# Optimization experiments

Hardware: AMD Instinct MI355X
Metric: run time of the kernel (lower is better)

## Reference

```python
import math
import jax, jax.numpy as jnp
import numpy as np

B, S, D, H = 2, 2048, 1024, 16
Dh = D // H
EPS = 1e-5


def layernorm(x, g, b):
    mu = jnp.mean(x, axis=-1, keepdims=True)
    var = jnp.mean(jnp.square(x - mu), axis=-1, keepdims=True)
    return (x - mu) * jax.lax.rsqrt(var + EPS) * g + b


def setup_inputs() -> dict:
    key = jax.random.key(0)
    ks = jax.random.split(key, 8)
    sc = 0.02
    return {
        "x": jax.random.normal(ks[0], (B, S, D), jnp.float32),
        # per-head wq weights stacked: [H, D, Dh] (wk/wv are unused in the original)
        "wq_w": jax.random.normal(ks[1], (H, D, Dh), jnp.float32) * sc,
        "wq_b": jnp.zeros((H, Dh), jnp.float32),
        "fc_w": jax.random.normal(ks[2], (D, D), jnp.float32) * sc,
        "fc_b": jnp.zeros((D,), jnp.float32),
        "ln1_g": jnp.ones((D,), jnp.float32),
        "ln1_b": jnp.zeros((D,), jnp.float32),
        "w1": jax.random.normal(ks[3], (D, 4 * D), jnp.float32) * sc,
        "b1": jnp.zeros((4 * D,), jnp.float32),
        "w2": jax.random.normal(ks[4], (4 * D, D), jnp.float32) * sc,
        "b2": jnp.zeros((D,), jnp.float32),
        "ln2_g": jnp.ones((D,), jnp.float32),
        "ln2_b": jnp.zeros((D,), jnp.float32),
    }


def reference(x, wq_w, wq_b, fc_w, fc_b, ln1_g, ln1_b, w1, b1, w2, b2, ln2_g, ln2_b):
    # NOTE: original bug — wq is applied to q, k and v; since q=k=v=x, Q=K=V.
    qh = jnp.einsum("bsd,hde->bhse", x, wq_w) + wq_b[None, :, None, :]  # [B,H,S,Dh]
    scores = jnp.einsum("bhse,bhte->bhst", qh, qh) / math.sqrt(Dh)      # [B,H,S,S]
    attn = jax.nn.softmax(scores, axis=-1)
    ctx = jnp.einsum("bhst,bhte->bhse", attn, qh)                        # [B,H,S,Dh]
    # concat heads along last dim (head h -> columns h*Dh:(h+1)*Dh)
    y = jnp.transpose(ctx, (0, 2, 1, 3)).reshape(B, S, D)
    y = y @ fc_w + fc_b
    y = layernorm(y + x, ln1_g, ln1_b)
    y1 = jax.nn.relu(y @ w1 + b1) @ w2 + b2
    return layernorm(y + y1, ln2_g, ln2_b)
```

## Files before the change

kernel.cpp:

```cpp
#include <hip/hip_runtime.h>
#include <hip/hip_bf16.h>

typedef unsigned short u16;
typedef __bf16 bf16x8 __attribute__((ext_vector_type(8)));
typedef float floatx4 __attribute__((ext_vector_type(4)));

__device__ __forceinline__ float bf2f_u(u16 u) {
    union { unsigned int i; float f; } x; x.i = ((unsigned int)u) << 16; return x.f;
}
__device__ __forceinline__ u16 f2bf_u(float f) {
    union { float f; unsigned int i; } x; x.f = f;
    unsigned int r = x.i + 0x7fffu + ((x.i >> 16) & 1u);
    return (u16)(r >> 16);
}

__device__ __forceinline__ void gl_lds16(const void* g, void* l) {
    __builtin_amdgcn_global_load_lds(
        (const __attribute__((address_space(1))) void*)g,
        (__attribute__((address_space(3))) void*)l, 16, 0, 0);
}

__global__ __launch_bounds__(256) void tobf_k(const float* __restrict__ in,
                                              u16* __restrict__ out) {
    int i = (blockIdx.x * 256 + threadIdx.x) * 8;
    float4 v0 = *(const float4*)&in[i];
    float4 v1 = *(const float4*)&in[i + 4];
    u16 tmp[8] = {f2bf_u(v0.x), f2bf_u(v0.y), f2bf_u(v0.z), f2bf_u(v0.w),
                  f2bf_u(v1.x), f2bf_u(v1.y), f2bf_u(v1.z), f2bf_u(v1.w)};
    *(uint4*)&out[i] = *(const uint4*)tmp;
}

__global__ __launch_bounds__(256) void transpose_bf_k(
    const float* __restrict__ in, u16* __restrict__ out,
    int R, int C, size_t inZ, size_t outZ)
{
    __shared__ u16 T[64][80];
    const float* ip = in + blockIdx.z * inZ;
    u16* op = out + blockIdx.z * outZ;
    const int r0 = blockIdx.y * 64, c0 = blockIdx.x * 64;
    const int t = threadIdx.x;
#pragma unroll
    for (int i = 0; i < 4; i++) {
        int c = t + i * 256;
        int rr = c >> 4, cc = (c & 15) * 4;
        float4 v = *(const float4*)&ip[(size_t)(r0 + rr) * C + c0 + cc];
        T[cc + 0][rr] = f2bf_u(v.x); T[cc + 1][rr] = f2bf_u(v.y);
        T[cc + 2][rr] = f2bf_u(v.z); T[cc + 3][rr] = f2bf_u(v.w);
    }
    __syncthreads();
#pragma unroll
    for (int i = 0; i < 2; i++) {
        int c = t + i * 256;
        int oc = c >> 3, k8 = (c & 7) * 8;
        uint4 v = *(const uint4*)&T[oc][k8];
        *(uint4*)&op[(size_t)(c0 + oc) * R + r0 + k8] = v;
    }
}

__global__ __launch_bounds__(256) void transpose_qh_k(const u16* __restrict__ in,
                                                      u16* __restrict__ out)
{
    __shared__ u16 T[64][72];
    const int bh = blockIdx.y;
    const int s0 = blockIdx.x * 64;
    const u16* ip = in + (size_t)bh * (2048 * 64);
    u16* op = out + (size_t)bh * (64 * 2048);
    const int t = threadIdx.x;
#pragma unroll
    for (int i = 0; i < 2; i++) {
        int c = t + i * 256;
        int r = c >> 3, cc = (c & 7) * 8;
        uint4 v = *(const uint4*)&ip[(size_t)(s0 + r) * 64 + cc];
        const u16* pv = (const u16*)&v;
#pragma unroll
        for (int k = 0; k < 8; k++) T[cc + k][r] = pv[k];
    }
    __syncthreads();
#pragma unroll
    for (int i = 0; i < 2; i++) {
        int c = t + i * 256;
        int d = c >> 3, cs = (c & 7) * 8;
        uint4 v = *(const uint4*)&T[d][cs];
        *(uint4*)&op[(size_t)d * 2048 + s0 + cs] = v;
    }
}

__device__ __forceinline__ void gemm_epilogue(
    floatx4 (&acc)[4][2], int m0, int n0, int wm, int wn, int lr, int quad,
    int N, const float* __restrict__ bias, const u16* __restrict__ resid,
    float* __restrict__ out, u16* __restrict__ out_bf, int mode)
{
#pragma unroll
    for (int i = 0; i < 4; i++) {
#pragma unroll
        for (int j = 0; j < 2; j++) {
#pragma unroll
            for (int r = 0; r < 4; r++) {
                int grow = m0 + wm + i * 16 + quad * 4 + r;
                int gcol = n0 + wn + j * 16 + lr;
                float val = acc[i][j][r];
                if (bias) val += bias[gcol];
                if (mode == 0) {
                    int bb = grow >> 11, ss = grow & 2047;
                    int h = gcol >> 6, e = gcol & 63;
                    out_bf[(((size_t)bb * 16 + h) * 2048 + ss) * 64 + e] = f2bf_u(val);
                } else if (mode == 1) {
                    size_t idx = (size_t)grow * N + gcol;
                    out[idx] = val + bf2f_u(resid[idx]);
                } else if (mode == 2) {
                    out_bf[(size_t)grow * N + gcol] = f2bf_u(fmaxf(val, 0.f));
                } else if (mode == 3) {
                    size_t idx = (size_t)grow * N + gcol;
                    out[idx] = out[idx] + val;
                } else {
                    size_t idx = (size_t)grow * N + gcol;
                    out_bf[idx] = f2bf_u(val + bf2f_u(resid[idx]));
                }
            }
        }
    }
}

__global__ __launch_bounds__(256) void gemm_bt64_k(
    const u16* __restrict__ A, const u16* __restrict__ Bt,
    int gm, int gn, int N, int K, int ldb,
    const float* __restrict__ bias, const u16* __restrict__ resid,
    float* __restrict__ out, u16* __restrict__ out_bf, int mode)
{
    __shared__ __align__(16) u16 As[2][128 * 64];
    __shared__ __align__(16) u16 Bs[2][64 * 64];

    const int id = blockIdx.x;
    const int xcd = id & 7, s = id >> 3;
    const int bandM = gm >> 2, bandN = gn >> 1;
    const int m0 = ((xcd >> 1) * bandM + (s % bandM)) * 128;
    const int n0 = ((xcd & 1) * bandN + (s / bandM)) * 64;

    const int t = threadIdx.x;
    const int wid = t >> 6, lane = t & 63;
    const int wm = (wid >> 1) * 64, wn = (wid & 1) * 32;
    const int lr = lane & 15, quad = lane >> 4;
    const int srow = lane >> 3;
    const int scol = ((lane & 7) ^ (lane >> 3)) * 8;

    floatx4 acc[4][2];
#pragma unroll
    for (int i = 0; i < 4; i++)
#pragma unroll
        for (int j = 0; j < 2; j++)
            acc[i][j] = (floatx4){0.f, 0.f, 0.f, 0.f};

    auto stage = [&](int b, int k0) {
#pragma unroll
        for (int i = 0; i < 4; i++) {
            int rb = wid * 32 + i * 8;
            gl_lds16(&A[(size_t)(m0 + rb + srow) * K + k0 + scol], &As[b][rb * 64]);
        }
#pragma unroll
        for (int i = 0; i < 2; i++) {
            int rb = wid * 16 + i * 8;
            gl_lds16(&Bt[(size_t)(n0 + rb + srow) * ldb + k0 + scol], &Bs[b][rb * 64]);
        }
    };

    const int nt = K >> 6;
    stage(0, 0);

    int cur = 0;
    for (int tt = 0; tt < nt; tt++) {
        asm volatile("s_waitcnt vmcnt(0)" ::: "memory");
        __builtin_amdgcn_s_barrier();
        __builtin_amdgcn_sched_barrier(0);
        if (tt + 1 < nt) stage(cur ^ 1, (tt + 1) * 64);

#pragma unroll
        for (int kk = 0; kk < 2; kk++) {
            bf16x8 af[4], bfr[2];
#pragma unroll
            for (int i = 0; i < 4; i++) {
                int R = wm + i * 16 + lr;
                int c = ((kk * 4 + quad) ^ (lr & 7)) * 8;
                af[i] = *(const bf16x8*)&As[cur][R * 64 + c];
            }
#pragma unroll
            for (int j = 0; j < 2; j++) {
                int R = wn + j * 16 + lr;
                int c = ((kk * 4 + quad) ^ (lr & 7)) * 8;
                bfr[j] = *(const bf16x8*)&Bs[cur][R * 64 + c];
            }
#pragma unroll
            for (int i = 0; i < 4; i++)
#pragma unroll
                for (int j = 0; j < 2; j++)
                    acc[i][j] = __builtin_amdgcn_mfma_f32_16x16x32_bf16(af[i], bfr[j], acc[i][j], 0, 0, 0);
        }
        cur ^= 1;
    }

    gemm_epilogue(acc, m0, n0, wm, wn, lr, quad, N, bias, resid, out, out_bf, mode);
}

__global__ __launch_bounds__(256) void gemm_bt64p3_k(
    const u16* __restrict__ A, const u16* __restrict__ Bt,
    int gm, int gn, int N, int K, int ldb,
    const float* __restrict__ bias, const u16* __restrict__ resid,
    float* __restrict__ out, u16* __restrict__ out_bf, int mode)
{
    __shared__ __align__(16) u16 As[3][128 * 64];
    __shared__ __align__(16) u16 Bs[3][64 * 64];

    const int id = blockIdx.x;
    const int xcd = id & 7, s = id >> 3;
    const int bandM = gm >> 2, bandN = gn >> 1;
    const int m0 = ((xcd >> 1) * bandM + (s % bandM)) * 128;
    const int n0 = ((xcd & 1) * bandN + (s / bandM)) * 64;

    const int t = threadIdx.x;
    const int wid = t >> 6, lane = t & 63;
    const int wm = (wid >> 1) * 64, wn = (wid & 1) * 32;
    const int lr = lane & 15, quad = lane >> 4;
    const int srow = lane >> 3;
    const int scol = ((lane & 7) ^ (lane >> 3)) * 8;

    floatx4 acc[4][2];
#pragma unroll
    for (int i = 0; i < 4; i++)
#pragma unroll
        for (int j = 0; j < 2; j++)
            acc[i][j] = (floatx4){0.f, 0.f, 0.f, 0.f};

    auto stage = [&](int b, int k0) {
#pragma unroll
        for (int i = 0; i < 4; i++) {
            int rb = wid * 32 + i * 8;
            gl_lds16(&A[(size_t)(m0 + rb + srow) * K + k0 + scol], &As[b][rb * 64]);
        }
#pragma unroll
        for (int i = 0; i < 2; i++) {
            int rb = wid * 16 + i * 8;
            gl_lds16(&Bt[(size_t)(n0 + rb + srow) * ldb + k0 + scol], &Bs[b][rb * 64]);
        }
    };

    const int nt = K >> 6;
    stage(0, 0);
    stage(1, 64);

    int cur = 0, nxt = 2;
    for (int tt = 0; tt < nt; tt++) {
        if (tt + 1 < nt) asm volatile("s_waitcnt vmcnt(6)" ::: "memory");
        else             asm volatile("s_waitcnt vmcnt(0)" ::: "memory");
        __builtin_amdgcn_s_barrier();
        __builtin_amdgcn_sched_barrier(0);
        if (tt + 2 < nt) stage(nxt, (tt + 2) * 64);

#pragma unroll
        for (int kk = 0; kk < 2; kk++) {
            bf16x8 af[4], bfr[2];
#pragma unroll
            for (int i = 0; i < 4; i++) {
                int R = wm + i * 16 + lr;
                int c = ((kk * 4 + quad) ^ (lr & 7)) * 8;
                af[i] = *(const bf16x8*)&As[cur][R * 64 + c];
            }
#pragma unroll
            for (int j = 0; j < 2; j++) {
                int R = wn + j * 16 + lr;
                int c = ((kk * 4 + quad) ^ (lr & 7)) * 8;
                bfr[j] = *(const bf16x8*)&Bs[cur][R * 64 + c];
            }
#pragma unroll
            for (int i = 0; i < 4; i++)
#pragma unroll
                for (int j = 0; j < 2; j++)
                    acc[i][j] = __builtin_amdgcn_mfma_f32_16x16x32_bf16(af[i], bfr[j], acc[i][j], 0, 0, 0);
        }
        cur = (cur == 2) ? 0 : cur + 1;
        nxt = (nxt == 2) ? 0 : nxt + 1;
    }

    gemm_epilogue(acc, m0, n0, wm, wn, lr, quad, N, bias, resid, out, out_bf, mode);
}

#define PST 68
__global__ __launch_bounds__(256) void attn_mfma_k(const u16* __restrict__ qh,
                                                   const u16* __restrict__ qhT,
                                                   u16* __restrict__ ctx)
{
    __shared__ __align__(16) u16 Ks[2][64 * 64];
    __shared__ __align__(16) u16 Vt[2][64 * 64];
    __shared__ __align__(16) u16 Ps[4][2][16][PST];

    const int bh = blockIdx.x >> 4;
    const int qb = blockIdx.x & 15;
    const u16* __restrict__ base  = qh  + (size_t)bh * (2048 * 64);
    const u16* __restrict__ baseT = qhT + (size_t)bh * (64 * 2048);
    const int t = threadIdx.x, wid = t >> 6, lane = t & 63;
    const int lr = lane & 15, quad = lane >> 4;
    const int q0 = qb * 128 + wid * 16;

    bf16x8 af[2][2];
#pragma unroll
    for (int f = 0; f < 2; f++) {
        af[f][0] = *(const bf16x8*)&base[(size_t)(q0 + f * 64 + lr) * 64 + quad * 8];
        af[f][1] = *(const bf16x8*)&base[(size_t)(q0 + f * 64 + lr) * 64 + quad * 8 + 32];
    }

    floatx4 Of[2][4];
#pragma unroll
    for (int f = 0; f < 2; f++)
#pragma unroll
        for (int dt = 0; dt < 4; dt++) Of[f][dt] = (floatx4){0.f, 0.f, 0.f, 0.f};
    float lsum[2] = {0.f, 0.f};

    const int srow = lane >> 3;
    const int schk = (lane & 7) ^ srow;

    auto stage = [&](int b, int kt) {
#pragma unroll
        for (int i = 0; i < 2; i++) {
            int rb = (wid * 2 + i) * 8;
            gl_lds16(&base[(size_t)(kt + rb + srow) * 64 + schk * 8],
                     &Ks[b][rb * 64]);
            gl_lds16(&baseT[(size_t)(rb + srow) * 2048 + kt + schk * 8],
                     &Vt[b][rb * 64]);
        }
    };

    stage(0, 0);
    __syncthreads();

    int buf = 0;
    for (int kt = 0; kt < 2048; kt += 64) {
        if (kt + 64 < 2048) stage(buf ^ 1, kt + 64);

#pragma unroll
        for (int nt = 0; nt < 4; nt++) {
            int row = nt * 16 + lr, rsw = row & 7;
            bf16x8 b0 = *(const bf16x8*)&Ks[buf][row * 64 + ((quad ^ rsw) * 8)];
            bf16x8 b1 = *(const bf16x8*)&Ks[buf][row * 64 + (((quad + 4) ^ rsw) * 8)];
#pragma unroll
            for (int f = 0; f < 2; f++) {
                floatx4 z = (floatx4){0.f, 0.f, 0.f, 0.f};
                z = __builtin_amdgcn_mfma_f32_16x16x32_bf16(b0, af[f][0], z, 0, 0, 0);
                z = __builtin_amdgcn_mfma_f32_16x16x32_bf16(b1, af[f][1], z, 0, 0, 0);
                float p0 = __expf(fminf(z[0] * 0.125f, 60.f));
                float p1 = __expf(fminf(z[1] * 0.125f, 60.f));
                float p2 = __expf(fminf(z[2] * 0.125f, 60.f));
                float p3 = __expf(fminf(z[3] * 0.125f, 60.f));
                lsum[f] += (p0 + p1) + (p2 + p3);
                unsigned int lo, hi;
                asm("v_cvt_pk_bf16_f32 %0, %1, %2" : "=v"(lo) : "v"(p0), "v"(p1));
                asm("v_cvt_pk_bf16_f32 %0, %1, %2" : "=v"(hi) : "v"(p2), "v"(p3));
                uint2 pk; pk.x = lo; pk.y = hi;
                *(uint2*)&Ps[wid][f][lr][nt * 16 + quad * 4] = pk;
            }
        }

        bf16x8 aP[2][2];
#pragma unroll
        for (int f = 0; f < 2; f++) {
            aP[f][0] = *(const bf16x8*)&Ps[wid][f][lr][quad * 8];
            aP[f][1] = *(const bf16x8*)&Ps[wid][f][lr][quad * 8 + 32];
        }
        __builtin_amdgcn_s_setprio(1);
#pragma unroll
        for (int dt = 0; dt < 4; dt++) {
            int d = dt * 16 + lr, dsw = d & 7;
            bf16x8 b0 = *(const bf16x8*)&Vt[buf][d * 64 + ((quad ^ dsw) * 8)];
            bf16x8 b1 = *(const bf16x8*)&Vt[buf][d * 64 + (((quad + 4) ^ dsw) * 8)];
#pragma unroll
            for (int f = 0; f < 2; f++) {
                Of[f][dt] = __builtin_amdgcn_mfma_f32_16x16x32_bf16(aP[f][0], b0, Of[f][dt], 0, 0, 0);
                Of[f][dt] = __builtin_amdgcn_mfma_f32_16x16x32_bf16(aP[f][1], b1, Of[f][dt], 0, 0, 0);
            }
        }
        __builtin_amdgcn_s_setprio(0);

        __syncthreads();
        buf ^= 1;
    }

    const int b = bh >> 4, h = bh & 15;
#pragma unroll
    for (int f = 0; f < 2; f++) {
        float l = lsum[f];
        l += __shfl_xor(l, 16);
        l += __shfl_xor(l, 32);
#pragma unroll
        for (int r = 0; r < 4; r++) {
            float lq = __shfl(l, quad * 4 + r);
            float inv = 1.f / lq;
            size_t rowoff = ((size_t)b * 2048 + q0 + f * 64 + quad * 4 + r) * 1024 + h * 64;
#pragma unroll
            for (int dt = 0; dt < 4; dt++)
                ctx[rowoff + dt * 16 + lr] = f2bf_u(Of[f][dt][r] * inv);
        }
    }
}

__global__ __launch_bounds__(256) void ln_k(const void* __restrict__ in,
                                            const float* __restrict__ g,
                                            const float* __restrict__ b,
                                            float* __restrict__ out_f,
                                            u16* __restrict__ out_bf, int icode)
{
    const int row = blockIdx.x;
    const int t = threadIdx.x;
    float4 v;
    if (icode) {
        v = *(const float4*)&((const float*)in)[(size_t)row * 1024 + t * 4];
    } else {
        ushort4 u = *(const ushort4*)&((const u16*)in)[(size_t)row * 1024 + t * 4];
        v.x = bf2f_u(u.x); v.y = bf2f_u(u.y); v.z = bf2f_u(u.z); v.w = bf2f_u(u.w);
    }
    float s  = v.x + v.y + v.z + v.w;
    float ss = v.x * v.x + v.y * v.y + v.z * v.z + v.w * v.w;
#pragma unroll
    for (int off = 32; off >= 1; off >>= 1) {
        s  += __shfl_down(s, off);
        ss += __shfl_down(ss, off);
    }
    __shared__ float sm[10];
    const int wid = t >> 6, lane = t & 63;
    if (lane == 0) { sm[wid] = s; sm[4 + wid] = ss; }
    __syncthreads();
    if (t == 0) {
        float S  = sm[0] + sm[1] + sm[2] + sm[3];
        float SS = sm[4] + sm[5] + sm[6] + sm[7];
        float mu = S * (1.f / 1024.f);
        float var = SS * (1.f / 1024.f) - mu * mu;
        sm[8] = mu; sm[9] = rsqrtf(fmaxf(var, 0.f) + 1e-5f);
    }
    __syncthreads();
    float mu = sm[8], rs = sm[9];
    float4 G  = *(const float4*)&g[t * 4];
    float4 Bv = *(const float4*)&b[t * 4];
    float r0 = (v.x - mu) * rs * G.x + Bv.x;
    float r1 = (v.y - mu) * rs * G.y + Bv.y;
    float r2 = (v.z - mu) * rs * G.z + Bv.z;
    float r3 = (v.w - mu) * rs * G.w + Bv.w;
    if (out_f) {
        float4 ov = {r0, r1, r2, r3};
        *(float4*)&out_f[(size_t)row * 1024 + t * 4] = ov;
    }
    if (out_bf) {
        ushort4 ou = {f2bf_u(r0), f2bf_u(r1), f2bf_u(r2), f2bf_u(r3)};
        *(ushort4*)&out_bf[(size_t)row * 1024 + t * 4] = ou;
    }
}

extern "C" void kernel_launch(void* const* d_in, const int* in_sizes, int n_in,
                              void* d_out, int out_size, void* d_ws, size_t ws_size,
                              hipStream_t stream)
{
    const float* x    = (const float*)d_in[0];
    const float* wq_w = (const float*)d_in[1];
    const float* wq_b = (const float*)d_in[2];
    const float* fc_w = (const float*)d_in[3];
    const float* fc_b = (const float*)d_in[4];
    const float* ln1g = (const float*)d_in[5];
    const float* ln1b = (const float*)d_in[6];
    const float* w1   = (const float*)d_in[7];
    const float* b1   = (const float*)d_in[8];
    const float* w2   = (const float*)d_in[9];
    const float* b2   = (const float*)d_in[10];
    const float* ln2g = (const float*)d_in[11];
    const float* ln2b = (const float*)d_in[12];

    char* ws = (char*)d_ws;
    const size_t MB = 1024 * 1024;
    u16*   w1_bt  = (u16*)(ws);
    u16*   w2_bt  = (u16*)(ws + 8 * MB);
    u16*   wqm_bt = (u16*)(ws + 16 * MB);
    u16*   fcw_bt = (u16*)(ws + 18 * MB);
    u16*   x_bf   = (u16*)(ws + 20 * MB);
    u16*   qh     = (u16*)(ws + 28 * MB);
    u16*   yln1   = (u16*)(ws + 28 * MB);
    u16*   ctx    = (u16*)(ws + 36 * MB);
    u16*   yfc_bf = (u16*)(ws + 44 * MB);
    u16*   qhT    = (u16*)(ws + 44 * MB);
    u16*   h1     = (u16*)(ws + 36 * MB);
    float* z      = (float*)d_out;
    const bool fullN = ws_size >= 69 * MB;

    transpose_bf_k<<<dim3(64, 16), 256, 0, stream>>>(w1, w1_bt, 1024, 4096, 0, 0);
    transpose_bf_k<<<dim3(16, 64), 256, 0, stream>>>(w2, w2_bt, 4096, 1024, 0, 0);
    transpose_bf_k<<<dim3(1, 16, 16), 256, 0, stream>>>(wq_w, wqm_bt, 1024, 64,
                                                        (size_t)1024 * 64, (size_t)64 * 1024);
    transpose_bf_k<<<dim3(16, 16), 256, 0, stream>>>(fc_w, fcw_bt, 1024, 1024, 0, 0);
    tobf_k<<<2048, 256, 0, stream>>>(x, x_bf);

    gemm_bt64p3_k<<<512, 256, 0, stream>>>(x_bf, wqm_bt, 32, 16, 1024, 1024, 1024,
                                           wq_b, nullptr, nullptr, qh, 0);
    transpose_qh_k<<<dim3(32, 32), 256, 0, stream>>>(qh, qhT);
    attn_mfma_k<<<512, 256, 0, stream>>>(qh, qhT, ctx);
    gemm_bt64p3_k<<<512, 256, 0, stream>>>(ctx, fcw_bt, 32, 16, 1024, 1024, 1024,
                                           fc_b, x_bf, nullptr, yfc_bf, 4);
    ln_k<<<4096, 256, 0, stream>>>(yfc_bf, ln1g, ln1b, nullptr, yln1, 0);

    if (fullN) {
        gemm_bt64_k<<<2048, 256, 0, stream>>>(yln1, w1_bt, 32, 64, 4096, 1024, 1024,
                                              b1, nullptr, nullptr, h1, 2);
        gemm_bt64p3_k<<<512, 256, 0, stream>>>(h1, w2_bt, 32, 16, 1024, 4096, 4096,
                                               b2, yln1, z, nullptr, 1);
    } else {
        gemm_bt64_k<<<1024, 256, 0, stream>>>(yln1, w1_bt, 32, 32, 2048, 1024, 1024,
                                              b1, nullptr, nullptr, h1, 2);
        gemm_bt64p3_k<<<512, 256, 0, stream>>>(h1, w2_bt, 32, 16, 1024, 2048, 4096,
                                               b2, yln1, z, nullptr, 1);
        gemm_bt64_k<<<1024, 256, 0, stream>>>(yln1, w1_bt + (size_t)2048 * 1024, 32, 32,
                                              2048, 1024, 1024,
                                              b1 + 2048, nullptr, nullptr, h1, 2);
        gemm_bt64p3_k<<<512, 256, 0, stream>>>(h1, w2_bt + 2048, 32, 16, 1024, 2048, 4096,
                                               nullptr, nullptr, z, nullptr, 3);
    }
    ln_k<<<4096, 256, 0, stream>>>(z, ln2g, ln2b, (float*)d_out, nullptr, 1);
}
```

Baseline: 388.8 us.

## Merge weight-prep launches and use 64x64-tile GEMM for FFN down-projection

Folds the four weight transposes and the x-to-bf16 conversion into one prep kernel that dispatches on block index, removing four launches. Adds a new GEMM kernel with 64x64 tiles, double-buffered LDS and XCD-aware tile mapping, and uses it for the w2 down-projection with 1024 blocks instead of 512. The smaller tiles give more parallelism for the K=4096 GEMM but less operand reuse per block and a shallower pipeline than the three-stage kernel.

After: 366.8 us. 1.06x faster.

```diff
diff --git a/kernel.cpp b/kernel.cpp
--- a/kernel.cpp
+++ b/kernel.cpp
@@ -20,25 +20,10 @@
         (__attribute__((address_space(3))) void*)l, 16, 0, 0);
 }
 
-__global__ __launch_bounds__(256) void tobf_k(const float* __restrict__ in,
-                                              u16* __restrict__ out) {
-    int i = (blockIdx.x * 256 + threadIdx.x) * 8;
-    float4 v0 = *(const float4*)&in[i];
-    float4 v1 = *(const float4*)&in[i + 4];
-    u16 tmp[8] = {f2bf_u(v0.x), f2bf_u(v0.y), f2bf_u(v0.z), f2bf_u(v0.w),
-                  f2bf_u(v1.x), f2bf_u(v1.y), f2bf_u(v1.z), f2bf_u(v1.w)};
-    *(uint4*)&out[i] = *(const uint4*)tmp;
-}
-
-__global__ __launch_bounds__(256) void transpose_bf_k(
-    const float* __restrict__ in, u16* __restrict__ out,
-    int R, int C, size_t inZ, size_t outZ)
-{
-    __shared__ u16 T[64][80];
-    const float* ip = in + blockIdx.z * inZ;
-    u16* op = out + blockIdx.z * outZ;
-    const int r0 = blockIdx.y * 64, c0 = blockIdx.x * 64;
-    const int t = threadIdx.x;
+__device__ __forceinline__ void transpose_body(
+    const float* __restrict__ ip, u16* __restrict__ op,
+    int R, int C, int r0, int c0, int t, u16 (*T)[80])
+{
 #pragma unroll
     for (int i = 0; i < 4; i++) {
         int c = t + i * 256;
@@ -54,6 +39,40 @@
         int oc = c >> 3, k8 = (c & 7) * 8;
         uint4 v = *(const uint4*)&T[oc][k8];
         *(uint4*)&op[(size_t)(c0 + oc) * R + r0 + k8] = v;
+    }
+}
+
+__global__ __launch_bounds__(256) void prep_k(
+    const float* __restrict__ x,    u16* __restrict__ x_bf,
+    const float* __restrict__ w1,   u16* __restrict__ w1_bt,
+    const float* __restrict__ w2,   u16* __restrict__ w2_bt,
+    const float* __restrict__ wq_w, u16* __restrict__ wqm_bt,
+    const float* __restrict__ fc_w, u16* __restrict__ fcw_bt)
+{
+    __shared__ u16 T[64][80];
+    const int id = blockIdx.x, t = threadIdx.x;
+    if (id < 2048) {
+        int i = (id * 256 + t) * 8;
+        float4 v0 = *(const float4*)&x[i];
+        float4 v1 = *(const float4*)&x[i + 4];
+        u16 tmp[8] = {f2bf_u(v0.x), f2bf_u(v0.y), f2bf_u(v0.z), f2bf_u(v0.w),
+                      f2bf_u(v1.x), f2bf_u(v1.y), f2bf_u(v1.z), f2bf_u(v1.w)};
+        *(uint4*)&x_bf[i] = *(const uint4*)tmp;
+    } else if (id < 3072) {
+        int j = id - 2048;
+        transpose_body(w1, w1_bt, 1024, 4096, (j >> 6) * 64, (j & 63) * 64, t, T);
+    } else if (id < 4096) {
+        int j = id - 3072;
+        transpose_body(w2, w2_bt, 4096, 1024, (j >> 4) * 64, (j & 15) * 64, t, T);
+    } else if (id < 4352) {
+        int j = id - 4096;
+        int z = j >> 4;
+        transpose_body(wq_w + (size_t)z * (1024 * 64),
+                       wqm_bt + (size_t)z * (64 * 1024),
+                       1024, 64, (j & 15) * 64, 0, t, T);
+    } else {
+        int j = id - 4352;
+        transpose_body(fc_w, fcw_bt, 1024, 1024, (j >> 4) * 64, (j & 15) * 64, t, T);
     }
 }
 
@@ -282,6 +301,106 @@
     gemm_epilogue(acc, m0, n0, wm, wn, lr, quad, N, bias, resid, out, out_bf, mode);
 }
 
+__global__ __launch_bounds__(256) void gemm_bt64m_k(
+    const u16* __restrict__ A, const u16* __restrict__ Bt,
+    int gm, int gn, int N, int K, int ldb,
+    const float* __restrict__ bias, const u16* __restrict__ resid,
+    float* __restrict__ out, u16* __restrict__ out_bf, int mode)
+{
+    __shared__ __align__(16) u16 As[2][64 * 64];
+    __shared__ __align__(16) u16 Bs[2][64 * 64];
+
+    const int id = blockIdx.x;
+    const int xcd = id & 7, s = id >> 3;
+    const int bandM = gm >> 2, bandN = gn >> 1;
+    const int m0 = ((xcd >> 1) * bandM + (s % bandM)) * 64;
+    const int n0 = ((xcd & 1) * bandN + (s / bandM)) * 64;
+
+    const int t = threadIdx.x;
+    const int wid = t >> 6, lane = t & 63;
+    const int wm = (wid >> 1) * 32, wn = (wid & 1) * 32;
+    const int lr = lane & 15, quad = lane >> 4;
+    const int srow = lane >> 3;
+    const int scol = ((lane & 7) ^ (lane >> 3)) * 8;
+
+    floatx4 acc[2][2];
+#pragma unroll
+    for (int i = 0; i < 2; i++)
+#pragma unroll
+        for (int j = 0; j < 2; j++)
+            acc[i][j] = (floatx4){0.f, 0.f, 0.f, 0.f};
+
+    auto stage = [&](int b, int k0) {
+#pragma unroll
+        for (int i = 0; i < 2; i++) {
+            int rb = wid * 16 + i * 8;
+            gl_lds16(&A[(size_t)(m0 + rb + srow) * K + k0 + scol], &As[b][rb * 64]);
+        }
+#pragma unroll
+        for (int i = 0; i < 2; i++) {
+            int rb = wid * 16 + i * 8;
+            gl_lds16(&Bt[(size_t)(n0 + rb + srow) * ldb + k0 + scol], &Bs[b][rb * 64]);
+        }
+    };
+
+    const int nt = K >> 6;
+    stage(0, 0);
+
+    int cur = 0;
+    for (int tt = 0; tt < nt; tt++) {
+        asm volatile("s_waitcnt vmcnt(0)" ::: "memory");
+        __builtin_amdgcn_s_barrier();
+        __builtin_amdgcn_sched_barrier(0);
+        if (tt + 1 < nt) stage(cur ^ 1, (tt + 1) * 64);
+
+#pragma unroll
+        for (int kk = 0; kk < 2; kk++) {
+            bf16x8 af[2], bfr[2];
+#pragma unroll
+            for (int i = 0; i < 2; i++) {
+                int R = wm + i * 16 + lr;
+                int c = ((kk * 4 + quad) ^ (lr & 7)) * 8;
+                af[i] = *(const bf16x8*)&As[cur][R * 64 + c];
+            }
+#pragma unroll
+            for (int j = 0; j < 2; j++) {
+                int R = wn + j * 16 + lr;
+                int c = ((kk * 4 + quad) ^ (lr & 7)) * 8;
+                bfr[j] = *(const bf16x8*)&Bs[cur][R * 64 + c];
+            }
+#pragma unroll
+            for (int i = 0; i < 2; i++)
+#pragma unroll
+                for (int j = 0; j < 2; j++)
+                    acc[i][j] = __builtin_amdgcn_mfma_f32_16x16x32_bf16(af[i], bfr[j], acc[i][j], 0, 0, 0);
+        }
+        cur ^= 1;
+    }
+
+#pragma unroll
+    for (int i = 0; i < 2; i++) {
+#pragma unroll
+        for (int j = 0; j < 2; j++) {
+#pragma unroll
+            for (int r = 0; r < 4; r++) {
+                int grow = m0 + wm + i * 16 + quad * 4 + r;
+                int gcol = n0 + wn + j * 16 + lr;
+                float val = acc[i][j][r];
+                if (bias) val += bias[gcol];
+                if (mode == 1) {
+                    size_t idx = (size_t)grow * N + gcol;
+                    out[idx] = val + bf2f_u(resid[idx]);
+                } else if (mode == 3) {
+                    size_t idx = (size_t)grow * N + gcol;
+                    out[idx] = out[idx] + val;
+                } else {
+                    out_bf[(size_t)grow * N + gcol] = f2bf_u(fmaxf(val, 0.f));
+                }
+            }
+        }
+    }
+}
+
 #define PST 68
 __global__ __launch_bounds__(256) void attn_mfma_k(const u16* __restrict__ qh,
                                                    const u16* __restrict__ qhT,
@@ -484,12 +603,8 @@
     float* z      = (float*)d_out;
     const bool fullN = ws_size >= 69 * MB;
 
-    transpose_bf_k<<<dim3(64, 16), 256, 0, stream>>>(w1, w1_bt, 1024, 4096, 0, 0);
-    transpose_bf_k<<<dim3(16, 64), 256, 0, stream>>>(w2, w2_bt, 4096, 1024, 0, 0);
-    transpose_bf_k<<<dim3(1, 16, 16), 256, 0, stream>>>(wq_w, wqm_bt, 1024, 64,
-                                                        (size_t)1024 * 64, (size_t)64 * 1024);
-    transpose_bf_k<<<dim3(16, 16), 256, 0, stream>>>(fc_w, fcw_bt, 1024, 1024, 0, 0);
-    tobf_k<<<2048, 256, 0, stream>>>(x, x_bf);
+    prep_k<<<4608, 256, 0, stream>>>(x, x_bf, w1, w1_bt, w2, w2_bt,
+                                     wq_w, wqm_bt, fc_w, fcw_bt);
 
     gemm_bt64p3_k<<<512, 256, 0, stream>>>(x_bf, wqm_bt, 32, 16, 1024, 1024, 1024,
                                            wq_b, nullptr, nullptr, qh, 0);
@@ -502,17 +617,17 @@
     if (fullN) {
         gemm_bt64_k<<<2048, 256, 0, stream>>>(yln1, w1_bt, 32, 64, 4096, 1024, 1024,
                                               b1, nullptr, nullptr, h1, 2);
-        gemm_bt64p3_k<<<512, 256, 0, stream>>>(h1, w2_bt, 32, 16, 1024, 4096, 4096,
+        gemm_bt64m_k<<<1024, 256, 0, stream>>>(h1, w2_bt, 64, 16, 1024, 4096, 4096,
                                                b2, yln1, z, nullptr, 1);
     } else {
         gemm_bt64_k<<<1024, 256, 0, stream>>>(yln1, w1_bt, 32, 32, 2048, 1024, 1024,
                                               b1, nullptr, nullptr, h1, 2);
-        gemm_bt64p3_k<<<512, 256, 0, stream>>>(h1, w2_bt, 32, 16, 1024, 2048, 4096,
+        gemm_bt64m_k<<<1024, 256, 0, stream>>>(h1, w2_bt, 64, 16, 1024, 2048, 4096,
                                                b2, yln1, z, nullptr, 1);
         gemm_bt64_k<<<1024, 256, 0, stream>>>(yln1, w1_bt + (size_t)2048 * 1024, 32, 32,
                                               2048, 1024, 1024,
                                               b1 + 2048, nullptr, nullptr, h1, 2);
-        gemm_bt64p3_k<<<512, 256, 0, stream>>>(h1, w2_bt + 2048, 32, 16, 1024, 2048, 4096,
+        gemm_bt64m_k<<<1024, 256, 0, stream>>>(h1, w2_bt + 2048, 64, 16, 1024, 2048, 4096,
                                                nullptr, nullptr, z, nullptr, 3);
     }
     ln_k<<<4096, 256, 0, stream>>>(z, ln2g, ln2b, (float*)d_out, nullptr, 1);
```
